# Kernel optimization log

Hardware: AMD Instinct MI355X
Metric: run time of the kernel (lower is better)

## Reference

```python
import jax, jax.numpy as jnp
import numpy as np

N = 100000   # nodes
E = 800000   # edges (avg degree 8)
D = 384      # feature dim (fixed by GraphConv(384,384))
OUT = 2      # out_channels


def setup_inputs() -> dict:
    key = jax.random.key(0)
    ks = jax.random.split(key, 10)
    s = 1.0 / np.sqrt(D)
    x = jax.random.normal(ks[0], (N, D), jnp.float32)
    edge_index = jax.random.randint(ks[1], (2, E), 0, N, dtype=jnp.int64)
    edge_weight = jax.random.uniform(ks[2], (E,), jnp.float32)
    return {
        "x": x,
        "edge_index": edge_index,
        "edge_weight": edge_weight,
        "W_rel1": jax.random.normal(ks[3], (D, D), jnp.float32) * s,
        "b_rel1": jnp.zeros((D,), jnp.float32),
        "W_root1": jax.random.normal(ks[4], (D, D), jnp.float32) * s,
        "W_rel2": jax.random.normal(ks[5], (D, D), jnp.float32) * s,
        "b_rel2": jnp.zeros((D,), jnp.float32),
        "W_root2": jax.random.normal(ks[6], (D, D), jnp.float32) * s,
        "W_lin": jax.random.normal(ks[7], (D, OUT), jnp.float32) * s,
        "b_lin": jnp.zeros((OUT,), jnp.float32),
    }


def _graph_conv(x, src, dst, ew, W_rel, b_rel, W_root):
    # PyG GraphConv (aggr='mean'): lin_rel(mean_j(ew_j * x_src_j)) + lin_root(x)
    msgs = ew[:, None] * x[src]                                   # [E, D] gather
    agg = jax.ops.segment_sum(msgs, dst, num_segments=N)          # [N, D] scatter
    cnt = jax.ops.segment_sum(jnp.ones_like(ew), dst, num_segments=N)
    mean = agg / jnp.maximum(cnt, 1.0)[:, None]
    return mean @ W_rel + b_rel + x @ W_root


def reference(x, edge_index, edge_weight,
              W_rel1, b_rel1, W_root1,
              W_rel2, b_rel2, W_root2,
              W_lin, b_lin):
    src, dst = edge_index[0], edge_index[1]
    h = jax.nn.relu(_graph_conv(x, src, dst, edge_weight, W_rel1, b_rel1, W_root1))
    # dropout(p=0.3) is identity in eval mode
    y = jax.nn.relu(_graph_conv(h, src, dst, edge_weight, W_rel2, b_rel2, W_root2))
    out = jax.nn.sigmoid(y @ W_lin + b_lin)                        # [N, OUT]
    return (out, y)
```

## Files before the change

### kernel.cpp

```cpp
#include <hip/hip_runtime.h>
#include <hip/hip_bf16.h>

typedef __bf16 bf16_t;
typedef bf16_t bf16x8 __attribute__((ext_vector_type(8)));
typedef float f32x4 __attribute__((ext_vector_type(4)));

typedef __attribute__((address_space(3))) unsigned int lds_u32;
typedef __attribute__((address_space(1))) unsigned int glb_u32;

__device__ __forceinline__ float bflo(unsigned int p){ union{unsigned int u; float f;} c; c.u = p << 16; return c.f; }
__device__ __forceinline__ float bfhi(unsigned int p){ union{unsigned int u; float f;} c; c.u = p & 0xffff0000u; return c.f; }
__device__ __forceinline__ unsigned int f2bfu(float f){
  union{float f; unsigned int u;} c; c.f = f;
  return (c.u + 0x7fffu + ((c.u >> 16) & 1u)) >> 16;
}

__global__ void k_cast_x(const float4* __restrict__ x, uint2* __restrict__ xb, int nq){
  int stride = gridDim.x * blockDim.x;
  for (int i = blockIdx.x * blockDim.x + threadIdx.x; i < nq; i += stride){
    float4 v = x[i];
    uint2 o;
    o.x = f2bfu(v.x) | (f2bfu(v.y) << 16);
    o.y = f2bfu(v.z) | (f2bfu(v.w) << 16);
    xb[i] = o;
  }
}

__global__ void k_castT_w4(const float* __restrict__ W0, const float* __restrict__ W1,
                           const float* __restrict__ W2, const float* __restrict__ W3,
                           unsigned short* __restrict__ T0, unsigned short* __restrict__ T1,
                           unsigned short* __restrict__ T2, unsigned short* __restrict__ T3){
  const float* W; unsigned short* T;
  switch (blockIdx.y){
    case 0: W = W0; T = T0; break;
    case 1: W = W1; T = T1; break;
    case 2: W = W2; T = T2; break;
    default: W = W3; T = T3; break;
  }
  int idx = blockIdx.x * 256 + threadIdx.x;
  int k = idx / 384, n = idx - k * 384;
  T[n * 384 + k] = (unsigned short)f2bfu(W[idx]);
}

__global__ void k_deg(const int* __restrict__ dst, int* __restrict__ deg, int E){
  int stride = gridDim.x * blockDim.x;
  for (int e = blockIdx.x * blockDim.x + threadIdx.x; e < E; e += stride)
    atomicAdd(&deg[dst[e]], 1);
}

__global__ void k_scan1(const int* __restrict__ deg, int* __restrict__ incl,
                        int* __restrict__ bsum, int n){
  __shared__ int wsum[16];
  int t = threadIdx.x, l = t & 63, w = t >> 6;
  int i = blockIdx.x * 1024 + t;
  int v = (i < n) ? deg[i] : 0;
  int xv = v;
  #pragma unroll
  for (int s = 1; s < 64; s <<= 1){
    int y = __shfl_up(xv, s, 64);
    if (l >= s) xv += y;
  }
  if (l == 63) wsum[w] = xv;
  __syncthreads();
  int off = 0;
  for (int k2 = 0; k2 < w; ++k2) off += wsum[k2];
  if (i < n) incl[i] = off + xv;
  if (t == 0){
    int tot = 0;
    for (int k2 = 0; k2 < 16; ++k2) tot += wsum[k2];
    bsum[blockIdx.x] = tot;
  }
}

__global__ void k_scan2(int* __restrict__ bsum, int nb){
  __shared__ int wtot;
  int t = threadIdx.x, l = t & 63, w = t >> 6;
  int v = (t < nb) ? bsum[t] : 0;
  int xv = v;
  #pragma unroll
  for (int s = 1; s < 64; s <<= 1){
    int y = __shfl_up(xv, s, 64);
    if (l >= s) xv += y;
  }
  if (t == 63) wtot = xv;
  __syncthreads();
  int off = (w == 1) ? wtot : 0;
  if (t < nb) bsum[t] = off + xv - v;
}

__global__ void k_scan3(const int* __restrict__ incl, const int* __restrict__ bsum,
                        const int* __restrict__ deg, int* __restrict__ rowptr,
                        int* __restrict__ cursor, int n){
  int i = blockIdx.x * 256 + threadIdx.x;
  if (i < n){
    int r = incl[i] + bsum[i >> 10];
    rowptr[i + 1] = r;
    cursor[i] = r - deg[i];
  }
  if (i == 0) rowptr[0] = 0;
}

__global__ void k_fill(const int* __restrict__ src, const int* __restrict__ dst, const float* __restrict__ ew,
                       int* __restrict__ cursor, int2* __restrict__ csr, int E){
  int stride = gridDim.x * blockDim.x;
  for (int e = blockIdx.x * blockDim.x + threadIdx.x; e < E; e += stride){
    int d = dst[e];
    int pos = atomicAdd(&cursor[d], 1);
    int2 c; c.x = src[e]; c.y = __float_as_int(ew[e]);
    csr[pos] = c;
  }
}

__global__ void k_agg(const unsigned short* __restrict__ X, unsigned short* __restrict__ OUT,
                      const int* __restrict__ rowptr, const int2* __restrict__ csr, int n_nodes){
  int w = threadIdx.x >> 6, l = threadIdx.x & 63;
  int node = blockIdx.x * 4 + w;
  if (node >= n_nodes) return;
  int e0 = rowptr[node], e1 = rowptr[node + 1];
  float a0=0,a1=0,a2=0,a3=0,a4=0,a5=0;
  const unsigned int* X32 = (const unsigned int*)X;
  int e = e0;
  for (; e + 2 <= e1; e += 2){
    int2 c0 = csr[e], c1 = csr[e + 1];
    const unsigned int* x0 = X32 + (long)c0.x * 192;
    const unsigned int* x1 = X32 + (long)c1.x * 192;
    unsigned int p0 = x0[l], p1 = x0[l + 64], p2 = x0[l + 128];
    unsigned int q0 = x1[l], q1 = x1[l + 64], q2 = x1[l + 128];
    float w0 = __int_as_float(c0.y), w1 = __int_as_float(c1.y);
    a0 += w0 * bflo(p0); a1 += w0 * bfhi(p0);
    a2 += w0 * bflo(p1); a3 += w0 * bfhi(p1);
    a4 += w0 * bflo(p2); a5 += w0 * bfhi(p2);
    a0 += w1 * bflo(q0); a1 += w1 * bfhi(q0);
    a2 += w1 * bflo(q1); a3 += w1 * bfhi(q1);
    a4 += w1 * bflo(q2); a5 += w1 * bfhi(q2);
  }
  if (e < e1){
    int2 c0 = csr[e];
    const unsigned int* x0 = X32 + (long)c0.x * 192;
    unsigned int p0 = x0[l], p1 = x0[l + 64], p2 = x0[l + 128];
    float w0 = __int_as_float(c0.y);
    a0 += w0 * bflo(p0); a1 += w0 * bfhi(p0);
    a2 += w0 * bflo(p1); a3 += w0 * bfhi(p1);
    a4 += w0 * bflo(p2); a5 += w0 * bfhi(p2);
  }
  int degn = e1 - e0;
  float inv = 1.0f / (float)(degn > 1 ? degn : 1);
  unsigned int* O32 = (unsigned int*)OUT + (long)node * 192;
  O32[l]       = f2bfu(a0 * inv) | (f2bfu(a1 * inv) << 16);
  O32[l + 64]  = f2bfu(a2 * inv) | (f2bfu(a3 * inv) << 16);
  O32[l + 128] = f2bfu(a4 * inv) | (f2bfu(a5 * inv) << 16);
}

template<int OUT_BF16>
__global__ __launch_bounds__(256) void k_gemm(
    const unsigned short* __restrict__ A1, const unsigned short* __restrict__ B1,
    const unsigned short* __restrict__ A2, const unsigned short* __restrict__ B2,
    const float* __restrict__ bias, void* __restrict__ Cout,
    const float* __restrict__ WL, float* __restrict__ olog,
    int NN, int q, int r)
{
  __shared__ __align__(16) unsigned short lsA[2 * 128 * 64];
  int t = threadIdx.x;
  int w = t >> 6, l = t & 63;

  int lin = blockIdx.x;
  int xcd = lin & 7, idx = lin >> 3;
  int nl = idx + ((xcd < r) ? xcd * (q + 1) : r * (q + 1) + (xcd - r) * q);
  int mt = nl / 3, nt = nl - mt * 3;
  int m0 = mt * 128, n0 = nt * 128;
  int wrow = (w & 1) * 64, wcol = (w >> 1) * 64;

  f32x4 acc[4][4] = {};

  int srow = t >> 3, sj = t & 7;
  int sjx = sj ^ (srow & 7);

  int rAb = wrow + (l & 15);
  int jx  = (l & 15) & 7;
  int kq  = l >> 4;
  int rB  = n0 + wcol + (l & 15);
  int koff = kq * 8;

#define STAGE(buf, kk_) do { \
    const unsigned short* Ag_ = ((kk_) < 6) ? A1 : A2; \
    int kc_ = (((kk_) < 6) ? (kk_) : (kk_) - 6) << 6; \
    _Pragma("unroll") \
    for (int p_ = 0; p_ < 4; ++p_){ \
      int ra_ = m0 + p_ * 32 + srow; if (ra_ >= NN) ra_ = NN - 1; \
      __builtin_amdgcn_global_load_lds((glb_u32*)(Ag_ + (long)ra_ * 384 + kc_ + sjx * 8), \
          (lds_u32*)((char*)lsA + (buf) * 16384 + p_ * 4096 + w * 1024), 16, 0, 0); \
    } \
  } while (0)

  STAGE(0, 0);

  #pragma unroll
  for (int kk = 0; kk < 12; ++kk){
    int cur = kk & 1;
    asm volatile("s_waitcnt vmcnt(0)" ::: "memory");
    asm volatile("s_barrier" ::: "memory");
    __builtin_amdgcn_sched_barrier(0);

    const unsigned short* Bg = (kk < 6) ? B1 : B2;
    int kc = ((kk < 6) ? kk : kk - 6) << 6;
    bf16x8 bfr[2][4];
    #pragma unroll
    for (int s = 0; s < 2; ++s)
      #pragma unroll
      for (int ni = 0; ni < 4; ++ni)
        bfr[s][ni] = *(const bf16x8*)&Bg[(long)(rB + ni * 16) * 384 + kc + s * 32 + koff];
    __builtin_amdgcn_sched_barrier(0);

    if (kk < 11) STAGE(cur ^ 1, kk + 1);
    __builtin_amdgcn_sched_barrier(0);

    const char* bA = (const char*)lsA + cur * 16384;
    #pragma unroll
    for (int s = 0; s < 2; ++s){
      bf16x8 af[4];
      #pragma unroll
      for (int mi = 0; mi < 4; ++mi)
        af[mi] = *(const bf16x8*)(bA + ((rAb + mi * 16) << 7) + ((((s << 2) + kq) ^ jx) << 4));
      #pragma unroll
      for (int mi = 0; mi < 4; ++mi)
        #pragma unroll
        for (int ni = 0; ni < 4; ++ni)
          acc[mi][ni] = __builtin_amdgcn_mfma_f32_16x16x32_bf16(af[mi], bfr[s][ni], acc[mi][ni], 0, 0, 0);
    }
  }
#undef STAGE

  int colb = l & 15;
  if (OUT_BF16){
    __syncthreads();
    unsigned short* lr = (unsigned short*)lsA;
    #pragma unroll
    for (int mi = 0; mi < 4; ++mi)
      #pragma unroll
      for (int ni = 0; ni < 4; ++ni){
        f32x4 v = acc[mi][ni];
        int col = wcol + ni * 16 + colb;
        float bcol = bias[n0 + col];
        #pragma unroll
        for (int rr = 0; rr < 4; ++rr){
          int row = wrow + mi * 16 + kq * 4 + rr;
          lr[row * 128 + col] = (unsigned short)f2bfu(fmaxf(v[rr] + bcol, 0.0f));
        }
      }
    __syncthreads();
    unsigned short* Cb = (unsigned short*)Cout;
    #pragma unroll
    for (int p = 0; p < 8; ++p){
      int idx16 = p * 256 + t;
      int row = idx16 >> 4, chunk = idx16 & 15;
      int rg = m0 + row;
      if (rg < NN)
        *(uint4*)((char*)Cb + (long)rg * 768 + n0 * 2 + chunk * 16) =
            *(const uint4*)((const char*)lsA + idx16 * 16);
    }
  } else {
    float* Cf = (float*)Cout;
    #pragma unroll
    for (int mi = 0; mi < 4; ++mi){
      float po[4][2] = {};
      #pragma unroll
      for (int ni = 0; ni < 4; ++ni){
        f32x4 v = acc[mi][ni];
        int col = n0 + wcol + ni * 16 + colb;
        float bcol = bias[col];
        float w0 = WL[col * 2], w1 = WL[col * 2 + 1];
        #pragma unroll
        for (int rr = 0; rr < 4; ++rr){
          int row = m0 + wrow + mi * 16 + kq * 4 + rr;
          float val = fmaxf(v[rr] + bcol, 0.0f);
          if (row < NN) Cf[(long)row * 384 + col] = val;
          po[rr][0] += val * w0;
          po[rr][1] += val * w1;
        }
      }
      #pragma unroll
      for (int rr = 0; rr < 4; ++rr)
        #pragma unroll
        for (int o = 0; o < 2; ++o){
          float v = po[rr][o];
          v += __shfl_xor(v, 1); v += __shfl_xor(v, 2);
          v += __shfl_xor(v, 4); v += __shfl_xor(v, 8);
          int row = m0 + wrow + mi * 16 + kq * 4 + rr;
          if (colb == 0 && row < NN) atomicAdd(&olog[row * 2 + o], v);
        }
    }
  }
}

__global__ void k_sig(const float* __restrict__ olog, const float* __restrict__ bl,
                      float* __restrict__ out, int n2){
  int i = blockIdx.x * 256 + threadIdx.x;
  if (i < n2) out[i] = 1.f / (1.f + expf(-(olog[i] + bl[i & 1])));
}

extern "C" void kernel_launch(void* const* d_in, const int* in_sizes, int n_in,
                              void* d_out, int out_size, void* d_ws, size_t ws_size,
                              hipStream_t stream) {
  const float* x      = (const float*)d_in[0];
  const int*   ei     = (const int*)d_in[1];
  const float* ew     = (const float*)d_in[2];
  const float* Wrel1  = (const float*)d_in[3];
  const float* brel1  = (const float*)d_in[4];
  const float* Wroot1 = (const float*)d_in[5];
  const float* Wrel2  = (const float*)d_in[6];
  const float* brel2  = (const float*)d_in[7];
  const float* Wroot2 = (const float*)d_in[8];
  const float* Wlin   = (const float*)d_in[9];
  const float* blin   = (const float*)d_in[10];

  const int NN = in_sizes[0] / 384;
  const int E  = in_sizes[2];
  const int* src = ei;
  const int* dst = ei + E;

  char* p = (char*)d_ws;
  auto carve = [&](size_t bytes) -> void* {
    void* r = (void*)p;
    p += (bytes + 255) & ~(size_t)255;
    return r;
  };
  int*   deg     = (int*)carve((size_t)NN * 4);
  int*   rowptr  = (int*)carve((size_t)(NN + 1) * 4);
  int*   cursor  = (int*)carve((size_t)NN * 4);
  int*   incl    = (int*)carve((size_t)NN * 4);
  int*   bsum    = (int*)carve(1024);
  float* olog    = (float*)carve((size_t)NN * 2 * 4);
  int2*  csr     = (int2*)carve((size_t)E * 8);
  unsigned short* xb  = (unsigned short*)carve((size_t)NN * 384 * 2);
  unsigned short* m1b = (unsigned short*)carve((size_t)NN * 384 * 2);
  unsigned short* hb  = (unsigned short*)carve((size_t)NN * 384 * 2);
  unsigned short* WT1 = (unsigned short*)carve(384 * 384 * 2);
  unsigned short* WT2 = (unsigned short*)carve(384 * 384 * 2);
  unsigned short* WT3 = (unsigned short*)carve(384 * 384 * 2);
  unsigned short* WT4 = (unsigned short*)carve(384 * 384 * 2);

  float* out = (float*)d_out;
  float* Y   = out + (size_t)NN * 2;

  int nScanB = (NN + 1023) / 1024;

  hipMemsetAsync(deg, 0, (size_t)NN * 4, stream);
  hipMemsetAsync(olog, 0, (size_t)NN * 8, stream);
  k_cast_x<<<2048, 256, 0, stream>>>((const float4*)x, (uint2*)xb, NN * 96);
  dim3 wg(576, 4);
  k_castT_w4<<<wg, 256, 0, stream>>>(Wrel1, Wroot1, Wrel2, Wroot2, WT1, WT2, WT3, WT4);
  k_deg<<<1024, 256, 0, stream>>>(dst, deg, E);
  k_scan1<<<nScanB, 1024, 0, stream>>>(deg, incl, bsum, NN);
  k_scan2<<<1, 128, 0, stream>>>(bsum, nScanB);
  k_scan3<<<(NN + 255) / 256, 256, 0, stream>>>(incl, bsum, deg, rowptr, cursor, NN);
  k_fill<<<1024, 256, 0, stream>>>(src, dst, ew, cursor, csr, E);

  int aggBlocks = (NN + 3) / 4;
  k_agg<<<aggBlocks, 256, 0, stream>>>(xb, m1b, rowptr, csr, NN);

  int nwg = 3 * ((NN + 127) / 128);
  int q = nwg >> 3, r = nwg & 7;
  k_gemm<1><<<nwg, 256, 0, stream>>>(m1b, WT1, xb, WT2, brel1, (void*)hb,
                                     nullptr, nullptr, NN, q, r);

  k_agg<<<aggBlocks, 256, 0, stream>>>(hb, m1b, rowptr, csr, NN);

  k_gemm<0><<<nwg, 256, 0, stream>>>(m1b, WT3, hb, WT4, brel2, (void*)Y,
                                     Wlin, olog, NN, q, r);

  k_sig<<<(NN * 2 + 255) / 256, 256, 0, stream>>>(olog, blin, out, NN * 2);
}
```

Measured before the change: 654.2 us.

## Load GEMM A operand directly into registers with double-buffered prefetch instead of LDS

The GEMM no longer stages A tiles through LDS with global_load_lds and per-k-step barriers. Each wave now loads its A and B fragments straight from global memory into registers, using a two-slot register buffer that prefetches the next k-step while MFMAs run on the current one. LDS is kept only for the bf16 epilogue. This removes the per-iteration waitcnt and barrier synchronisation, but each wave now fetches its own A rows from global memory without sharing them across waves, and register pressure goes up, which can reduce occupancy.

```diff
diff --git a/kernel.cpp b/kernel.cpp
--- a/kernel.cpp
+++ b/kernel.cpp
@@ -4,9 +4,6 @@
 typedef __bf16 bf16_t;
 typedef bf16_t bf16x8 __attribute__((ext_vector_type(8)));
 typedef float f32x4 __attribute__((ext_vector_type(4)));
-
-typedef __attribute__((address_space(3))) unsigned int lds_u32;
-typedef __attribute__((address_space(1))) unsigned int glb_u32;
 
 __device__ __forceinline__ float bflo(unsigned int p){ union{unsigned int u; float f;} c; c.u = p << 16; return c.f; }
 __device__ __forceinline__ float bfhi(unsigned int p){ union{unsigned int u; float f;} c; c.u = p & 0xffff0000u; return c.f; }
@@ -159,7 +156,7 @@
     const float* __restrict__ WL, float* __restrict__ olog,
     int NN, int q, int r)
 {
-  __shared__ __align__(16) unsigned short lsA[2 * 128 * 64];
+  __shared__ __align__(16) unsigned short lsE[OUT_BF16 ? 128 * 128 : 64];
   int t = threadIdx.x;
   int w = t >> 6, l = t & 63;
 
@@ -170,70 +167,81 @@
   int m0 = mt * 128, n0 = nt * 128;
   int wrow = (w & 1) * 64, wcol = (w >> 1) * 64;
 
+  int colb = l & 15, kq = l >> 4;
+
   f32x4 acc[4][4] = {};
 
-  int srow = t >> 3, sj = t & 7;
-  int sjx = sj ^ (srow & 7);
-
-  int rAb = wrow + (l & 15);
-  int jx  = (l & 15) & 7;
-  int kq  = l >> 4;
-  int rB  = n0 + wcol + (l & 15);
-  int koff = kq * 8;
-
-#define STAGE(buf, kk_) do { \
-    const unsigned short* Ag_ = ((kk_) < 6) ? A1 : A2; \
-    int kc_ = (((kk_) < 6) ? (kk_) : (kk_) - 6) << 6; \
-    _Pragma("unroll") \
-    for (int p_ = 0; p_ < 4; ++p_){ \
-      int ra_ = m0 + p_ * 32 + srow; if (ra_ >= NN) ra_ = NN - 1; \
-      __builtin_amdgcn_global_load_lds((glb_u32*)(Ag_ + (long)ra_ * 384 + kc_ + sjx * 8), \
-          (lds_u32*)((char*)lsA + (buf) * 16384 + p_ * 4096 + w * 1024), 16, 0, 0); \
-    } \
-  } while (0)
-
-  STAGE(0, 0);
+  const unsigned short* pA[4];
+  const unsigned short* pB[4];
+  #pragma unroll
+  for (int mi = 0; mi < 4; ++mi){
+    int rA = m0 + wrow + mi * 16 + colb; if (rA >= NN) rA = NN - 1;
+    pA[mi] = A1 + (long)rA * 384 + kq * 8;
+  }
+  #pragma unroll
+  for (int ni = 0; ni < 4; ++ni){
+    int rB = n0 + wcol + ni * 16 + colb;
+    pB[ni] = B1 + (long)rB * 384 + kq * 8;
+  }
+  const long dA = A2 - A1, dB = B2 - B1;
+
+  bf16x8 afb[2][2][4];
+  bf16x8 bfb[2][4];
+
+  #pragma unroll
+  for (int s = 0; s < 2; ++s)
+    #pragma unroll
+    for (int mi = 0; mi < 4; ++mi)
+      afb[0][s][mi] = *(const bf16x8*)(pA[mi] + s * 32);
+  #pragma unroll
+  for (int ni = 0; ni < 4; ++ni)
+    bfb[0][ni] = *(const bf16x8*)(pB[ni]);
 
   #pragma unroll
   for (int kk = 0; kk < 12; ++kk){
-    int cur = kk & 1;
-    asm volatile("s_waitcnt vmcnt(0)" ::: "memory");
-    asm volatile("s_barrier" ::: "memory");
-    __builtin_amdgcn_sched_barrier(0);
-
-    const unsigned short* Bg = (kk < 6) ? B1 : B2;
-    int kc = ((kk < 6) ? kk : kk - 6) << 6;
-    bf16x8 bfr[2][4];
-    #pragma unroll
-    for (int s = 0; s < 2; ++s)
+    const int cur = kk & 1;
+    const int kc  = (kk < 6 ? kk : kk - 6) * 64;
+
+    if (kk == 5){
+      #pragma unroll
+      for (int mi = 0; mi < 4; ++mi) pA[mi] += dA;
+    }
+    if (kk < 11){
+      const int kc2 = ((kk + 1) < 6 ? (kk + 1) : (kk + 1) - 6) * 64;
+      #pragma unroll
+      for (int s = 0; s < 2; ++s)
+        #pragma unroll
+        for (int mi = 0; mi < 4; ++mi)
+          afb[cur ^ 1][s][mi] = *(const bf16x8*)(pA[mi] + kc2 + s * 32);
+    }
+    #pragma unroll
+    for (int ni = 0; ni < 4; ++ni)
+      bfb[1][ni] = *(const bf16x8*)(pB[ni] + kc + 32);
+    #pragma unroll
+    for (int mi = 0; mi < 4; ++mi)
       #pragma unroll
       for (int ni = 0; ni < 4; ++ni)
-        bfr[s][ni] = *(const bf16x8*)&Bg[(long)(rB + ni * 16) * 384 + kc + s * 32 + koff];
-    __builtin_amdgcn_sched_barrier(0);
-
-    if (kk < 11) STAGE(cur ^ 1, kk + 1);
-    __builtin_amdgcn_sched_barrier(0);
-
-    const char* bA = (const char*)lsA + cur * 16384;
-    #pragma unroll
-    for (int s = 0; s < 2; ++s){
-      bf16x8 af[4];
-      #pragma unroll
-      for (int mi = 0; mi < 4; ++mi)
-        af[mi] = *(const bf16x8*)(bA + ((rAb + mi * 16) << 7) + ((((s << 2) + kq) ^ jx) << 4));
-      #pragma unroll
-      for (int mi = 0; mi < 4; ++mi)
-        #pragma unroll
-        for (int ni = 0; ni < 4; ++ni)
-          acc[mi][ni] = __builtin_amdgcn_mfma_f32_16x16x32_bf16(af[mi], bfr[s][ni], acc[mi][ni], 0, 0, 0);
-    }
-  }
-#undef STAGE
-
-  int colb = l & 15;
+        acc[mi][ni] = __builtin_amdgcn_mfma_f32_16x16x32_bf16(afb[cur][0][mi], bfb[0][ni], acc[mi][ni], 0, 0, 0);
+
+    if (kk == 5){
+      #pragma unroll
+      for (int ni = 0; ni < 4; ++ni) pB[ni] += dB;
+    }
+    if (kk < 11){
+      const int kc2 = ((kk + 1) < 6 ? (kk + 1) : (kk + 1) - 6) * 64;
+      #pragma unroll
+      for (int ni = 0; ni < 4; ++ni)
+        bfb[0][ni] = *(const bf16x8*)(pB[ni] + kc2);
+    }
+    #pragma unroll
+    for (int mi = 0; mi < 4; ++mi)
+      #pragma unroll
+      for (int ni = 0; ni < 4; ++ni)
+        acc[mi][ni] = __builtin_amdgcn_mfma_f32_16x16x32_bf16(afb[cur][1][mi], bfb[1][ni], acc[mi][ni], 0, 0, 0);
+  }
+
   if (OUT_BF16){
     __syncthreads();
-    unsigned short* lr = (unsigned short*)lsA;
     #pragma unroll
     for (int mi = 0; mi < 4; ++mi)
       #pragma unroll
@@ -244,7 +252,7 @@
         #pragma unroll
         for (int rr = 0; rr < 4; ++rr){
           int row = wrow + mi * 16 + kq * 4 + rr;
-          lr[row * 128 + col] = (unsigned short)f2bfu(fmaxf(v[rr] + bcol, 0.0f));
+          lsE[row * 128 + col] = (unsigned short)f2bfu(fmaxf(v[rr] + bcol, 0.0f));
         }
       }
     __syncthreads();
@@ -256,7 +264,7 @@
       int rg = m0 + row;
       if (rg < NN)
         *(uint4*)((char*)Cb + (long)rg * 768 + n0 * 2 + chunk * 16) =
-            *(const uint4*)((const char*)lsA + idx16 * 16);
+            *(const uint4*)((const char*)lsE + idx16 * 16);
     }
   } else {
     float* Cf = (float*)Cout;
```

Result: slower. 844.0 us (+29.0%).

## Reorder GraphConv as transform-then-aggregate and fuse epilogue into aggregation

Applied to the files above, without the earlier changes.

Uses linearity to compute P = X·W_rel and R = X·W_root first in one dual-output GEMM, then aggregates the transformed rows P over edges and adds R, bias and ReLU inside the aggregation kernel. The final layer's aggregation also writes Y in fp32 and computes the linear head plus sigmoid in-kernel, which removes the atomic logit buffer, its memset and the separate sigmoid launch. The GEMM now reads a single A operand, and h overwrites xb in place. The trade-off is an extra bf16 rounding of P before aggregation and an extra N×D intermediate (R) written and read per layer.

```diff
diff --git a/kernel.cpp b/kernel.cpp
--- a/kernel.cpp
+++ b/kernel.cpp
@@ -111,19 +111,137 @@
   }
 }
 
-__global__ void k_agg(const unsigned short* __restrict__ X, unsigned short* __restrict__ OUT,
-                      const int* __restrict__ rowptr, const int2* __restrict__ csr, int n_nodes){
+__global__ __launch_bounds__(256) void k_gemm_dual(
+    const unsigned short* __restrict__ A, const unsigned short* __restrict__ B1,
+    const unsigned short* __restrict__ B2,
+    unsigned short* __restrict__ P, unsigned short* __restrict__ R,
+    int NN, int q, int r)
+{
+  __shared__ __align__(16) unsigned short lds[2 * 128 * 32 * 2];
+  int t = threadIdx.x, w = t >> 6, l = t & 63;
+
+  int lin = blockIdx.x, xcd = lin & 7, idx = lin >> 3;
+  int nl = idx + ((xcd < r) ? xcd * (q + 1) : r * (q + 1) + (xcd - r) * q);
+  int mt = nl / 3, nt = nl - mt * 3;
+  int m0 = mt * 128, n0 = nt * 128;
+  int wrow = (w & 1) * 64, wcol = (w >> 1) * 64;
+  int colb = l & 15, kq = l >> 4;
+
+  f32x4 accP[4][4] = {}, accR[4][4] = {};
+
+  int gchunk = (l & 3) ^ ((l >> 3) & 3);
+
+  const unsigned short* pB2[4];
+  #pragma unroll
+  for (int ni = 0; ni < 4; ++ni)
+    pB2[ni] = B2 + (long)(n0 + wcol + ni * 16 + colb) * 384 + kq * 8;
+
+  bf16x8 b2r[2][4];
+
+#define STAGE(buf, kk_) do { \
+    int kc_ = (kk_) * 32; \
+    _Pragma("unroll") \
+    for (int q2 = 0; q2 < 2; ++q2){ \
+      int rt = (q2 * 4 + w) * 16 + (l >> 2); \
+      int ra = m0 + rt; if (ra >= NN) ra = NN - 1; \
+      __builtin_amdgcn_global_load_lds((glb_u32*)(A + (long)ra * 384 + kc_ + gchunk * 8), \
+          (lds_u32*)((char*)lds + (buf) * 8192 + (q2 * 4 + w) * 1024), 16, 0, 0); \
+      __builtin_amdgcn_global_load_lds((glb_u32*)(B1 + (long)(n0 + rt) * 384 + kc_ + gchunk * 8), \
+          (lds_u32*)((char*)lds + 16384 + (buf) * 8192 + (q2 * 4 + w) * 1024), 16, 0, 0); \
+    } \
+  } while (0)
+
+  STAGE(0, 0);
+  #pragma unroll
+  for (int ni = 0; ni < 4; ++ni)
+    b2r[0][ni] = *(const bf16x8*)(pB2[ni]);
+  __syncthreads();
+
+  #pragma unroll
+  for (int kk = 0; kk < 12; ++kk){
+    const int cur = kk & 1;
+
+    if (kk < 11){
+      #pragma unroll
+      for (int ni = 0; ni < 4; ++ni)
+        b2r[cur ^ 1][ni] = *(const bf16x8*)(pB2[ni] + (kk + 1) * 32);
+      STAGE(cur ^ 1, kk + 1);
+    }
+
+    const char* bA = (const char*)lds + cur * 8192;
+    const char* bB = (const char*)lds + 16384 + cur * 8192;
+    bf16x8 af[4], b1f[4];
+    #pragma unroll
+    for (int mi = 0; mi < 4; ++mi){
+      int rA = wrow + mi * 16 + colb;
+      af[mi] = *(const bf16x8*)(bA + rA * 64 + ((kq ^ ((rA >> 1) & 3)) << 4));
+    }
+    #pragma unroll
+    for (int ni = 0; ni < 4; ++ni){
+      int rB = wcol + ni * 16 + colb;
+      b1f[ni] = *(const bf16x8*)(bB + rB * 64 + ((kq ^ ((rB >> 1) & 3)) << 4));
+    }
+    #pragma unroll
+    for (int mi = 0; mi < 4; ++mi)
+      #pragma unroll
+      for (int ni = 0; ni < 4; ++ni){
+        accP[mi][ni] = __builtin_amdgcn_mfma_f32_16x16x32_bf16(af[mi], b1f[ni], accP[mi][ni], 0, 0, 0);
+        accR[mi][ni] = __builtin_amdgcn_mfma_f32_16x16x32_bf16(af[mi], b2r[cur][ni], accR[mi][ni], 0, 0, 0);
+      }
+
+    __syncthreads();
+  }
+#undef STAGE
+
+  unsigned short* lr = (unsigned short*)lds;
+  #pragma unroll
+  for (int pass = 0; pass < 2; ++pass){
+    __syncthreads();
+    #pragma unroll
+    for (int mi = 0; mi < 4; ++mi)
+      #pragma unroll
+      for (int ni = 0; ni < 4; ++ni){
+        f32x4 v = pass ? accR[mi][ni] : accP[mi][ni];
+        int col = wcol + ni * 16 + colb;
+        #pragma unroll
+        for (int rr = 0; rr < 4; ++rr){
+          int row = wrow + mi * 16 + kq * 4 + rr;
+          lr[row * 128 + col] = (unsigned short)f2bfu(v[rr]);
+        }
+      }
+    __syncthreads();
+    unsigned short* O = pass ? R : P;
+    #pragma unroll
+    for (int p = 0; p < 8; ++p){
+      int idx16 = p * 256 + t;
+      int row = idx16 >> 4, chunk = idx16 & 15;
+      int rg = m0 + row;
+      if (rg < NN)
+        *(uint4*)(O + (long)rg * 384 + n0 + chunk * 8) =
+            *(const uint4*)((const char*)lds + idx16 * 16);
+    }
+  }
+}
+
+template<int FINAL>
+__global__ void k_agg2(const unsigned short* __restrict__ Pm, const unsigned short* __restrict__ Rm,
+                       const float* __restrict__ bias,
+                       const int* __restrict__ rowptr, const int2* __restrict__ csr,
+                       unsigned short* __restrict__ hout,
+                       float* __restrict__ Y, const float* __restrict__ WL,
+                       const float* __restrict__ bl, float* __restrict__ outp,
+                       int n_nodes){
   int w = threadIdx.x >> 6, l = threadIdx.x & 63;
   int node = blockIdx.x * 4 + w;
   if (node >= n_nodes) return;
   int e0 = rowptr[node], e1 = rowptr[node + 1];
   float a0=0,a1=0,a2=0,a3=0,a4=0,a5=0;
-  const unsigned int* X32 = (const unsigned int*)X;
+  const unsigned int* P32 = (const unsigned int*)Pm;
   int e = e0;
   for (; e + 2 <= e1; e += 2){
     int2 c0 = csr[e], c1 = csr[e + 1];
-    const unsigned int* x0 = X32 + (long)c0.x * 192;
-    const unsigned int* x1 = X32 + (long)c1.x * 192;
+    const unsigned int* x0 = P32 + (long)c0.x * 192;
+    const unsigned int* x1 = P32 + (long)c1.x * 192;
     unsigned int p0 = x0[l], p1 = x0[l + 64], p2 = x0[l + 128];
     unsigned int q0 = x1[l], q1 = x1[l + 64], q2 = x1[l + 128];
     float w0 = __int_as_float(c0.y), w1 = __int_as_float(c1.y);
@@ -136,7 +254,7 @@
   }
   if (e < e1){
     int2 c0 = csr[e];
-    const unsigned int* x0 = X32 + (long)c0.x * 192;
+    const unsigned int* x0 = P32 + (long)c0.x * 192;
     unsigned int p0 = x0[l], p1 = x0[l + 64], p2 = x0[l + 128];
     float w0 = __int_as_float(c0.y);
     a0 += w0 * bflo(p0); a1 += w0 * bfhi(p0);
@@ -145,157 +263,43 @@
   }
   int degn = e1 - e0;
   float inv = 1.0f / (float)(degn > 1 ? degn : 1);
-  unsigned int* O32 = (unsigned int*)OUT + (long)node * 192;
-  O32[l]       = f2bfu(a0 * inv) | (f2bfu(a1 * inv) << 16);
-  O32[l + 64]  = f2bfu(a2 * inv) | (f2bfu(a3 * inv) << 16);
-  O32[l + 128] = f2bfu(a4 * inv) | (f2bfu(a5 * inv) << 16);
-}
-
-template<int OUT_BF16>
-__global__ __launch_bounds__(256) void k_gemm(
-    const unsigned short* __restrict__ A1, const unsigned short* __restrict__ B1,
-    const unsigned short* __restrict__ A2, const unsigned short* __restrict__ B2,
-    const float* __restrict__ bias, void* __restrict__ Cout,
-    const float* __restrict__ WL, float* __restrict__ olog,
-    int NN, int q, int r)
-{
-  __shared__ __align__(16) unsigned short lsA[2 * 128 * 64];
-  int t = threadIdx.x;
-  int w = t >> 6, l = t & 63;
-
-  int lin = blockIdx.x;
-  int xcd = lin & 7, idx = lin >> 3;
-  int nl = idx + ((xcd < r) ? xcd * (q + 1) : r * (q + 1) + (xcd - r) * q);
-  int mt = nl / 3, nt = nl - mt * 3;
-  int m0 = mt * 128, n0 = nt * 128;
-  int wrow = (w & 1) * 64, wcol = (w >> 1) * 64;
-
-  f32x4 acc[4][4] = {};
-
-  int srow = t >> 3, sj = t & 7;
-  int sjx = sj ^ (srow & 7);
-
-  int rAb = wrow + (l & 15);
-  int jx  = (l & 15) & 7;
-  int kq  = l >> 4;
-  int rB  = n0 + wcol + (l & 15);
-  int koff = kq * 8;
-
-#define STAGE(buf, kk_) do { \
-    const unsigned short* Ag_ = ((kk_) < 6) ? A1 : A2; \
-    int kc_ = (((kk_) < 6) ? (kk_) : (kk_) - 6) << 6; \
-    _Pragma("unroll") \
-    for (int p_ = 0; p_ < 4; ++p_){ \
-      int ra_ = m0 + p_ * 32 + srow; if (ra_ >= NN) ra_ = NN - 1; \
-      __builtin_amdgcn_global_load_lds((glb_u32*)(Ag_ + (long)ra_ * 384 + kc_ + sjx * 8), \
-          (lds_u32*)((char*)lsA + (buf) * 16384 + p_ * 4096 + w * 1024), 16, 0, 0); \
-    } \
-  } while (0)
-
-  STAGE(0, 0);
-
-  #pragma unroll
-  for (int kk = 0; kk < 12; ++kk){
-    int cur = kk & 1;
-    asm volatile("s_waitcnt vmcnt(0)" ::: "memory");
-    asm volatile("s_barrier" ::: "memory");
-    __builtin_amdgcn_sched_barrier(0);
-
-    const unsigned short* Bg = (kk < 6) ? B1 : B2;
-    int kc = ((kk < 6) ? kk : kk - 6) << 6;
-    bf16x8 bfr[2][4];
-    #pragma unroll
-    for (int s = 0; s < 2; ++s)
-      #pragma unroll
-      for (int ni = 0; ni < 4; ++ni)
-        bfr[s][ni] = *(const bf16x8*)&Bg[(long)(rB + ni * 16) * 384 + kc + s * 32 + koff];
-    __builtin_amdgcn_sched_barrier(0);
-
-    if (kk < 11) STAGE(cur ^ 1, kk + 1);
-    __builtin_amdgcn_sched_barrier(0);
-
-    const char* bA = (const char*)lsA + cur * 16384;
-    #pragma unroll
-    for (int s = 0; s < 2; ++s){
-      bf16x8 af[4];
-      #pragma unroll
-      for (int mi = 0; mi < 4; ++mi)
-        af[mi] = *(const bf16x8*)(bA + ((rAb + mi * 16) << 7) + ((((s << 2) + kq) ^ jx) << 4));
-      #pragma unroll
-      for (int mi = 0; mi < 4; ++mi)
-        #pragma unroll
-        for (int ni = 0; ni < 4; ++ni)
-          acc[mi][ni] = __builtin_amdgcn_mfma_f32_16x16x32_bf16(af[mi], bfr[s][ni], acc[mi][ni], 0, 0, 0);
-    }
-  }
-#undef STAGE
-
-  int colb = l & 15;
-  if (OUT_BF16){
-    __syncthreads();
-    unsigned short* lr = (unsigned short*)lsA;
-    #pragma unroll
-    for (int mi = 0; mi < 4; ++mi)
-      #pragma unroll
-      for (int ni = 0; ni < 4; ++ni){
-        f32x4 v = acc[mi][ni];
-        int col = wcol + ni * 16 + colb;
-        float bcol = bias[n0 + col];
-        #pragma unroll
-        for (int rr = 0; rr < 4; ++rr){
-          int row = wrow + mi * 16 + kq * 4 + rr;
-          lr[row * 128 + col] = (unsigned short)f2bfu(fmaxf(v[rr] + bcol, 0.0f));
-        }
-      }
-    __syncthreads();
-    unsigned short* Cb = (unsigned short*)Cout;
-    #pragma unroll
-    for (int p = 0; p < 8; ++p){
-      int idx16 = p * 256 + t;
-      int row = idx16 >> 4, chunk = idx16 & 15;
-      int rg = m0 + row;
-      if (rg < NN)
-        *(uint4*)((char*)Cb + (long)rg * 768 + n0 * 2 + chunk * 16) =
-            *(const uint4*)((const char*)lsA + idx16 * 16);
-    }
+
+  const unsigned int* R32 = (const unsigned int*)Rm + (long)node * 192;
+  unsigned int r0 = R32[l], r1 = R32[l + 64], r2 = R32[l + 128];
+  const float2* bias2 = (const float2*)bias;
+  float2 b0 = bias2[l], b1 = bias2[l + 64], b2 = bias2[l + 128];
+
+  float h0 = fmaxf(a0 * inv + bflo(r0) + b0.x, 0.0f);
+  float h1 = fmaxf(a1 * inv + bfhi(r0) + b0.y, 0.0f);
+  float h2 = fmaxf(a2 * inv + bflo(r1) + b1.x, 0.0f);
+  float h3 = fmaxf(a3 * inv + bfhi(r1) + b1.y, 0.0f);
+  float h4 = fmaxf(a4 * inv + bflo(r2) + b2.x, 0.0f);
+  float h5 = fmaxf(a5 * inv + bfhi(r2) + b2.y, 0.0f);
+
+  if (!FINAL){
+    unsigned int* O32 = (unsigned int*)hout + (long)node * 192;
+    O32[l]       = f2bfu(h0) | (f2bfu(h1) << 16);
+    O32[l + 64]  = f2bfu(h2) | (f2bfu(h3) << 16);
+    O32[l + 128] = f2bfu(h4) | (f2bfu(h5) << 16);
   } else {
-    float* Cf = (float*)Cout;
-    #pragma unroll
-    for (int mi = 0; mi < 4; ++mi){
-      float po[4][2] = {};
-      #pragma unroll
-      for (int ni = 0; ni < 4; ++ni){
-        f32x4 v = acc[mi][ni];
-        int col = n0 + wcol + ni * 16 + colb;
-        float bcol = bias[col];
-        float w0 = WL[col * 2], w1 = WL[col * 2 + 1];
-        #pragma unroll
-        for (int rr = 0; rr < 4; ++rr){
-          int row = m0 + wrow + mi * 16 + kq * 4 + rr;
-          float val = fmaxf(v[rr] + bcol, 0.0f);
-          if (row < NN) Cf[(long)row * 384 + col] = val;
-          po[rr][0] += val * w0;
-          po[rr][1] += val * w1;
-        }
-      }
-      #pragma unroll
-      for (int rr = 0; rr < 4; ++rr)
-        #pragma unroll
-        for (int o = 0; o < 2; ++o){
-          float v = po[rr][o];
-          v += __shfl_xor(v, 1); v += __shfl_xor(v, 2);
-          v += __shfl_xor(v, 4); v += __shfl_xor(v, 8);
-          int row = m0 + wrow + mi * 16 + kq * 4 + rr;
-          if (colb == 0 && row < NN) atomicAdd(&olog[row * 2 + o], v);
-        }
-    }
-  }
-}
-
-__global__ void k_sig(const float* __restrict__ olog, const float* __restrict__ bl,
-                      float* __restrict__ out, int n2){
-  int i = blockIdx.x * 256 + threadIdx.x;
-  if (i < n2) out[i] = 1.f / (1.f + expf(-(olog[i] + bl[i & 1])));
+    float2* Y2 = (float2*)Y + (long)node * 192;
+    Y2[l]       = make_float2(h0, h1);
+    Y2[l + 64]  = make_float2(h2, h3);
+    Y2[l + 128] = make_float2(h4, h5);
+    const float4* WL4 = (const float4*)WL;
+    float4 w0 = WL4[l], w1 = WL4[l + 64], w2 = WL4[l + 128];
+    float s0 = h0 * w0.x + h1 * w0.z + h2 * w1.x + h3 * w1.z + h4 * w2.x + h5 * w2.z;
+    float s1 = h0 * w0.y + h1 * w0.w + h2 * w1.y + h3 * w1.w + h4 * w2.y + h5 * w2.w;
+    #pragma unroll
+    for (int m = 32; m; m >>= 1){
+      s0 += __shfl_xor(s0, m);
+      s1 += __shfl_xor(s1, m);
+    }
+    if (l == 0){
+      outp[(long)node * 2]     = 1.f / (1.f + expf(-(s0 + bl[0])));
+      outp[(long)node * 2 + 1] = 1.f / (1.f + expf(-(s1 + bl[1])));
+    }
+  }
 }
 
 extern "C" void kernel_launch(void* const* d_in, const int* in_sizes, int n_in,
@@ -329,11 +333,10 @@
   int*   cursor  = (int*)carve((size_t)NN * 4);
   int*   incl    = (int*)carve((size_t)NN * 4);
   int*   bsum    = (int*)carve(1024);
-  float* olog    = (float*)carve((size_t)NN * 2 * 4);
   int2*  csr     = (int2*)carve((size_t)E * 8);
-  unsigned short* xb  = (unsigned short*)carve((size_t)NN * 384 * 2);
-  unsigned short* m1b = (unsigned short*)carve((size_t)NN * 384 * 2);
-  unsigned short* hb  = (unsigned short*)carve((size_t)NN * 384 * 2);
+  unsigned short* xb = (unsigned short*)carve((size_t)NN * 384 * 2);
+  unsigned short* Pb = (unsigned short*)carve((size_t)NN * 384 * 2);
+  unsigned short* Rb = (unsigned short*)carve((size_t)NN * 384 * 2);
   unsigned short* WT1 = (unsigned short*)carve(384 * 384 * 2);
   unsigned short* WT2 = (unsigned short*)carve(384 * 384 * 2);
   unsigned short* WT3 = (unsigned short*)carve(384 * 384 * 2);
@@ -345,7 +348,6 @@
   int nScanB = (NN + 1023) / 1024;
 
   hipMemsetAsync(deg, 0, (size_t)NN * 4, stream);
-  hipMemsetAsync(olog, 0, (size_t)NN * 8, stream);
   k_cast_x<<<2048, 256, 0, stream>>>((const float4*)x, (uint2*)xb, NN * 96);
   dim3 wg(576, 4);
   k_castT_w4<<<wg, 256, 0, stream>>>(Wrel1, Wroot1, Wrel2, Wroot2, WT1, WT2, WT3, WT4);
@@ -355,18 +357,15 @@
   k_scan3<<<(NN + 255) / 256, 256, 0, stream>>>(incl, bsum, deg, rowptr, cursor, NN);
   k_fill<<<1024, 256, 0, stream>>>(src, dst, ew, cursor, csr, E);
 
-  int aggBlocks = (NN + 3) / 4;
-  k_agg<<<aggBlocks, 256, 0, stream>>>(xb, m1b, rowptr, csr, NN);
-
   int nwg = 3 * ((NN + 127) / 128);
   int q = nwg >> 3, r = nwg & 7;
-  k_gemm<1><<<nwg, 256, 0, stream>>>(m1b, WT1, xb, WT2, brel1, (void*)hb,
-                                     nullptr, nullptr, NN, q, r);
-
-  k_agg<<<aggBlocks, 256, 0, stream>>>(hb, m1b, rowptr, csr, NN);
-
-  k_gemm<0><<<nwg, 256, 0, stream>>>(m1b, WT3, hb, WT4, brel2, (void*)Y,
-                                     Wlin, olog, NN, q, r);
-
-  k_sig<<<(NN * 2 + 255) / 256, 256, 0, stream>>>(olog, blin, out, NN * 2);
-}
+  int aggBlocks = (NN + 3) / 4;
+
+  k_gemm_dual<<<nwg, 256, 0, stream>>>(xb, WT1, WT2, Pb, Rb, NN, q, r);
+  k_agg2<0><<<aggBlocks, 256, 0, stream>>>(Pb, Rb, brel1, rowptr, csr,
+                                           xb, nullptr, nullptr, nullptr, nullptr, NN);
+
+  k_gemm_dual<<<nwg, 256, 0, stream>>>(xb, WT3, WT4, Pb, Rb, NN, q, r);
+  k_agg2<1><<<aggBlocks, 256, 0, stream>>>(Pb, Rb, brel2, rowptr, csr,
+                                           nullptr, Y, Wlin, blin, out, NN);
+}
```

Measured after the change: 649.5 us. About the same (-0.7%).
